# Kernel tuning notes

Hardware: AMD Instinct MI355X
Metric: run time of the kernel (lower is better)

## Reference

```python
import jax, jax.numpy as jnp
import numpy as np

B = 64; H = 56; W = 56; C = 128; NH = 4; WS = 7; SHIFT = 3; HID = 512
N = WS * WS            # tokens per window = 49
NW = (H // WS) * (W // WS)  # windows per image = 64
HD = C // NH           # head dim = 32


def _rel_index():
    # standard Swin relative-position index, [N, N] in [0, (2*WS-1)^2)
    coords = np.stack(np.meshgrid(np.arange(WS), np.arange(WS), indexing='ij'))  # [2,WS,WS]
    cf = coords.reshape(2, -1)
    rel = (cf[:, :, None] - cf[:, None, :]).transpose(1, 2, 0).astype(np.int64)  # [N,N,2]
    rel[:, :, 0] += WS - 1
    rel[:, :, 1] += WS - 1
    rel[:, :, 0] *= 2 * WS - 1
    return rel.sum(-1).astype(np.int32)


def _attn_mask():
    # standard Swin shifted-window mask, [NW, N, N] with 0 / -100
    img = np.zeros((H, W))
    cnt = 0
    sl = (slice(0, -WS), slice(-WS, -SHIFT), slice(-SHIFT, None))
    for hs in sl:
        for ws_ in sl:
            img[hs, ws_] = cnt
            cnt += 1
    mw = img.reshape(H // WS, WS, W // WS, WS).transpose(0, 2, 1, 3).reshape(-1, N)
    diff = mw[:, None, :] - mw[:, :, None]
    return np.where(diff != 0, -100.0, 0.0).astype(np.float32)


def setup_inputs() -> dict:
    key = jax.random.key(0)
    ks = jax.random.split(key, 12)
    s = 0.02
    return {
        'x': jax.random.normal(ks[0], (B, H * W, C), jnp.float32),
        'g1': jnp.ones((C,), jnp.float32),
        'b1': jnp.zeros((C,), jnp.float32),
        'w_qkv': jax.random.normal(ks[1], (C, 3 * C), jnp.float32) * s,
        'b_qkv': jnp.zeros((3 * C,), jnp.float32),
        'rel_bias': jax.random.normal(ks[2], ((2 * WS - 1) ** 2, NH), jnp.float32) * s,
        'w_proj': jax.random.normal(ks[3], (C, C), jnp.float32) * s,
        'b_proj': jnp.zeros((C,), jnp.float32),
        'g2': jnp.ones((C,), jnp.float32),
        'b2': jnp.zeros((C,), jnp.float32),
        'w_in': jax.random.normal(ks[4], (C, 2 * HID), jnp.float32) * s,
        'b_in': jnp.zeros((2 * HID,), jnp.float32),
        'w_core': jax.random.normal(ks[5], (HID, C), jnp.float32) * s,
        'b_core': jnp.zeros((C,), jnp.float32),
        'attn_mask': jnp.asarray(_attn_mask()),
        'rel_index': jnp.asarray(_rel_index()),
    }


def _ln(x, g, b, eps=1e-5):
    m = jnp.mean(x, axis=-1, keepdims=True)
    v = jnp.mean(jnp.square(x - m), axis=-1, keepdims=True)
    return (x - m) * jax.lax.rsqrt(v + eps) * g + b


def reference(x, g1, b1, w_qkv, b_qkv, rel_bias, w_proj, b_proj,
              g2, b2, w_in, b_in, w_core, b_core, attn_mask, rel_index):
    shortcut = x
    y = _ln(x, g1, b1).reshape(B, H, W, C)
    # cyclic shift
    y = jnp.roll(y, (-SHIFT, -SHIFT), axis=(1, 2))
    # window partition -> [B*NW, N, C]
    win = y.reshape(B, H // WS, WS, W // WS, WS, C).transpose(0, 1, 3, 2, 4, 5)
    win = win.reshape(B * NW, N, C)
    # qkv
    qkv = (win @ w_qkv + b_qkv).reshape(B * NW, N, 3, NH, HD).transpose(2, 0, 3, 1, 4)
    q, k, v = qkv[0], qkv[1], qkv[2]           # each [B*NW, NH, N, HD]
    scale = HD ** -0.5
    attn = jnp.einsum('bhqd,bhkd->bhqk', q * scale, k)   # [B*NW, NH, N, N]
    bias = rel_bias[rel_index]                  # [N, N, NH]
    attn = attn + bias.transpose(2, 0, 1)[None]
    # shifted-window mask
    attn = attn.reshape(B, NW, NH, N, N) + attn_mask[None, :, None]
    attn = jax.nn.softmax(attn.reshape(B * NW, NH, N, N), axis=-1)
    o = jnp.einsum('bhqk,bhkd->bhqd', attn, v).transpose(0, 2, 1, 3).reshape(B * NW, N, C)
    o = o @ w_proj + b_proj
    # window reverse + un-shift
    o = o.reshape(B, H // WS, W // WS, WS, WS, C).transpose(0, 1, 3, 2, 4, 5).reshape(B, H, W, C)
    o = jnp.roll(o, (SHIFT, SHIFT), axis=(1, 2)).reshape(B, H * W, C)
    x = shortcut + o
    # TM feed-forward (geglu gate path, continuous relaxation of the TM core)
    y = _ln(x, g2, b2)
    p = y @ w_in + b_in
    val, gate = jnp.split(p, 2, axis=-1)
    fused = jax.nn.gelu(val) * jax.nn.sigmoid(gate)
    out = fused @ w_core + b_core
    return x + out
```

## Files before the change

kernel.cpp:

```cpp
#include <hip/hip_runtime.h>
#include <hip/hip_bf16.h>


typedef unsigned short u16;
typedef __attribute__((ext_vector_type(8))) short short8;
typedef __attribute__((ext_vector_type(4))) float f32x4;

#define T_TOK 200704
#define CDIM  128
#define NTOK  49
#define WSZ   7
#define SHIFT 3
#define HID   512
#define PAD   136

__device__ __forceinline__ float bf2f(u16 v) {
    return __uint_as_float(((unsigned int)v) << 16);
}
__device__ __forceinline__ u16 f2bf(float f) {
    unsigned int u = __float_as_uint(f);
    unsigned int r = 0x7FFFu + ((u >> 16) & 1u);
    return (u16)((u + r) >> 16);
}

__global__ __launch_bounds__(256) void prep_weights(
    const float* __restrict__ w_qkv, const float* __restrict__ w_proj,
    const float* __restrict__ w_in,  const float* __restrict__ w_core,
    u16* __restrict__ qkvT, u16* __restrict__ projT,
    u16* __restrict__ inT,  u16* __restrict__ coreT)
{
    int g = blockIdx.x * 256 + threadIdx.x;
    if (g < 49152) {
        int k = g / 384, n = g % 384;
        qkvT[n * 128 + k] = f2bf(w_qkv[g]);
    } else if (g < 65536) {
        int h = g - 49152; int k = h / 128, n = h % 128;
        projT[n * 128 + k] = f2bf(w_proj[h]);
    } else if (g < 196608) {
        int h = g - 65536; int k = h / 1024, n = h % 1024;
        inT[n * 128 + k] = f2bf(w_in[h]);
    } else {
        int h = g - 196608; int k = h / 128, n = h % 128;
        coreT[n * 512 + k] = f2bf(w_core[h]);
    }
}

__global__ __launch_bounds__(256) void prep_combo(
    const float* __restrict__ mask, const float* __restrict__ rel_bias,
    const int* __restrict__ rel_index, u16* __restrict__ combo)
{
    int g = blockIdx.x * 256 + threadIdx.x;
    if (g >= 64 * 4 * 49 * 64) return;
    int kj = g & 63;
    int qi = (g >> 6) % 49;
    int head = (g / (64 * 49)) & 3;
    int w = g / (64 * 49 * 4);
    float v = 0.f;
    if (kj < 49) {
        int e = qi * 49 + kj;
        v = mask[w * 2401 + e] + rel_bias[rel_index[e] * 4 + head];
    }
    combo[g] = f2bf(v);
}

__global__ __launch_bounds__(256) void ln1_kernel(
    const float* __restrict__ xin, const float* __restrict__ gam,
    const float* __restrict__ bet, u16* __restrict__ outp)
{
    int wave = threadIdx.x >> 6, lane = threadIdx.x & 63;
    int t = blockIdx.x * 4 + wave;
    int win = t / NTOK, n = t - win * NTOK;
    int b = win >> 6, wi = win & 63;
    int hp = (wi >> 3) * WSZ + n / WSZ;
    int wp = (wi & 7) * WSZ + n % WSZ;
    int h = hp + SHIFT; if (h >= 56) h -= 56;
    int w = wp + SHIFT; if (w >= 56) w -= 56;
    int src = b * 3136 + h * 56 + w;
    const float* xr = xin + (size_t)src * CDIM;
    int c0 = lane * 2;
    float x0 = xr[c0], x1 = xr[c0 + 1];
    float s = x0 + x1;
    #pragma unroll
    for (int m = 1; m < 64; m <<= 1) s += __shfl_xor(s, m);
    float mean = s * (1.0f / 128.0f);
    float d0 = x0 - mean, d1 = x1 - mean;
    float v = d0 * d0 + d1 * d1;
    #pragma unroll
    for (int m = 1; m < 64; m <<= 1) v += __shfl_xor(v, m);
    float rstd = rsqrtf(v * (1.0f / 128.0f) + 1e-5f);
    float y0 = d0 * rstd * gam[c0]     + bet[c0];
    float y1 = d1 * rstd * gam[c0 + 1] + bet[c0 + 1];
    u16 pair[2] = { f2bf(y0), f2bf(y1) };
    *(unsigned int*)(outp + (size_t)t * CDIM + c0) = *(unsigned int*)pair;
}

__global__ __launch_bounds__(256) void ln2_kernel(
    const u16* __restrict__ xin, const float* __restrict__ gam,
    const float* __restrict__ bet, u16* __restrict__ outp)
{
    int wave = threadIdx.x >> 6, lane = threadIdx.x & 63;
    int t = blockIdx.x * 4 + wave;
    const u16* xr = xin + (size_t)t * CDIM;
    int c0 = lane * 2;
    float x0 = bf2f(xr[c0]), x1 = bf2f(xr[c0 + 1]);
    float s = x0 + x1;
    #pragma unroll
    for (int m = 1; m < 64; m <<= 1) s += __shfl_xor(s, m);
    float mean = s * (1.0f / 128.0f);
    float d0 = x0 - mean, d1 = x1 - mean;
    float v = d0 * d0 + d1 * d1;
    #pragma unroll
    for (int m = 1; m < 64; m <<= 1) v += __shfl_xor(v, m);
    float rstd = rsqrtf(v * (1.0f / 128.0f) + 1e-5f);
    float y0 = d0 * rstd * gam[c0]     + bet[c0];
    float y1 = d1 * rstd * gam[c0 + 1] + bet[c0 + 1];
    u16 pair[2] = { f2bf(y0), f2bf(y1) };
    *(unsigned int*)(outp + (size_t)t * CDIM + c0) = *(unsigned int*)pair;
}

__global__ __launch_bounds__(256) void qkv_gemm(
    const u16* __restrict__ A, const u16* __restrict__ WT,
    const float* __restrict__ bias,
    u16* __restrict__ qb, u16* __restrict__ kb, u16* __restrict__ vb)
{
    __shared__ __align__(16) short As[128 * PAD];
    __shared__ __align__(16) short Bs[64 * PAD];
    int tid = threadIdx.x;
    int m0 = blockIdx.x * 128;
    #pragma unroll
    for (int i = 0; i < 8; i++) {
        int e = i * 256 + tid; int row = e >> 4, c = e & 15;
        *(int4*)(As + row * PAD + c * 8) =
            *(const int4*)(A + (size_t)(m0 + row) * 128 + c * 8);
    }
    int w = tid >> 6, lane = tid & 63, lr = lane & 15, quad = lane >> 4;
    short8 af[2][4];
    const float scale = 0.17677669529663687f;
    for (int n0 = 0; n0 < 6; n0++) {
        #pragma unroll
        for (int i = 0; i < 4; i++) {
            int e = i * 256 + tid; int row = e >> 4, c = e & 15;
            *(int4*)(Bs + row * PAD + c * 8) =
                *(const int4*)(WT + (size_t)(n0 * 64 + row) * 128 + c * 8);
        }
        __syncthreads();
        if (n0 == 0) {
            #pragma unroll
            for (int mr = 0; mr < 2; mr++)
                #pragma unroll
                for (int ks = 0; ks < 4; ks++)
                    af[mr][ks] = *(const short8*)(As + (mr * 64 + w * 16 + lr) * PAD + ks * 32 + quad * 8);
        }
        f32x4 acc[8];
        #pragma unroll
        for (int i = 0; i < 8; i++) acc[i] = (f32x4){0.f, 0.f, 0.f, 0.f};
        #pragma unroll
        for (int ks = 0; ks < 4; ks++) {
            #pragma unroll
            for (int nt = 0; nt < 4; nt++) {
                short8 b = *(const short8*)(Bs + (nt * 16 + lr) * PAD + ks * 32 + quad * 8);
                acc[nt]     = __builtin_amdgcn_mfma_f32_16x16x32_bf16(af[0][ks], b, acc[nt], 0, 0, 0);
                acc[4 + nt] = __builtin_amdgcn_mfma_f32_16x16x32_bf16(af[1][ks], b, acc[4 + nt], 0, 0, 0);
            }
        }
        __syncthreads();
        #pragma unroll
        for (int nt = 0; nt < 4; nt++) {
            int col = n0 * 64 + nt * 16 + lr;
            int which = col >> 7, head = (col >> 5) & 3, hd = col & 31;
            u16* dst = (which == 0) ? qb : (which == 1 ? kb : vb);
            float bv = bias[col];
            #pragma unroll
            for (int mr = 0; mr < 2; mr++) {
                #pragma unroll
                for (int r = 0; r < 4; r++) {
                    int m = m0 + mr * 64 + w * 16 + quad * 4 + r;
                    int win = m / NTOK, n = m - win * NTOK;
                    float v = acc[mr * 4 + nt][r] + bv;
                    if (which == 0) v *= scale;
                    dst[(size_t)((win * 4 + head) * NTOK + n) * 32 + hd] = f2bf(v);
                }
            }
        }
    }
}

__global__ __launch_bounds__(256) void attn_kernel(
    const u16* __restrict__ qb, const u16* __restrict__ kb,
    const u16* __restrict__ vb, const u16* __restrict__ combo,
    u16* __restrict__ ob)
{
    __shared__ __align__(16) short Ps[4][64 * 72];
    __shared__ __align__(16) short Vt[4][32 * 72];
    int win = blockIdx.x;
    int w = threadIdx.x >> 6;
    int lane = threadIdx.x & 63;
    int lr = lane & 15, quad = lane >> 4;
    int wh = win * 4 + w;
    const u16* qp = qb + (size_t)wh * 1568;
    const u16* kp = kb + (size_t)wh * 1568;

    {
        const unsigned int* vp = (const unsigned int*)(vb + (size_t)wh * 1568);
        short* vt = Vt[w];
        for (int u = lane; u < 784; u += 64) {
            unsigned int v2 = vp[u];
            int kj = u >> 4, hd2 = (u & 15) * 2;
            vt[hd2 * 72 + kj]       = (short)(v2 & 0xffff);
            vt[(hd2 + 1) * 72 + kj] = (short)(v2 >> 16);
        }
    }

    short8 qa[4], kf[4];
    #pragma unroll
    for (int t = 0; t < 4; t++) {
        int row = t * 16 + lr;
        if (row < 49) {
            qa[t] = *(const short8*)(qp + row * 32 + quad * 8);
            kf[t] = *(const short8*)(kp + row * 32 + quad * 8);
        } else {
            qa[t] = (short8){0,0,0,0,0,0,0,0};
            kf[t] = (short8){0,0,0,0,0,0,0,0};
        }
    }

    f32x4 s[4][4];
    #pragma unroll
    for (int mt = 0; mt < 4; mt++)
        #pragma unroll
        for (int nt = 0; nt < 4; nt++)
            s[mt][nt] = (f32x4){0.f, 0.f, 0.f, 0.f};
    #pragma unroll
    for (int mt = 0; mt < 4; mt++)
        #pragma unroll
        for (int nt = 0; nt < 4; nt++)
            s[mt][nt] = __builtin_amdgcn_mfma_f32_16x16x32_bf16(qa[mt], kf[nt], s[mt][nt], 0, 0, 0);

    const u16* cb = combo + (size_t)(((win & 63) * 4 + w) * 49) * 64;
    short* ps = Ps[w];
    #pragma unroll
    for (int mt = 0; mt < 4; mt++) {
        #pragma unroll
        for (int r = 0; r < 4; r++) {
            int qi = mt * 16 + quad * 4 + r;
            float vv[4];
            #pragma unroll
            for (int nt = 0; nt < 4; nt++) {
                int kj = nt * 16 + lr;
                float val = s[mt][nt][r];
                if (kj < 49) {
                    if (qi < 49) val += bf2f(cb[qi * 64 + kj]);
                } else {
                    val = -1e30f;
                }
                vv[nt] = val;
            }
            float mx = fmaxf(fmaxf(vv[0], vv[1]), fmaxf(vv[2], vv[3]));
            #pragma unroll
            for (int msk = 1; msk < 16; msk <<= 1) mx = fmaxf(mx, __shfl_xor(mx, msk));
            float e[4], sum = 0.f;
            #pragma unroll
            for (int nt = 0; nt < 4; nt++) { e[nt] = __expf(vv[nt] - mx); sum += e[nt]; }
            #pragma unroll
            for (int msk = 1; msk < 16; msk <<= 1) sum += __shfl_xor(sum, msk);
            float inv = 1.f / sum;
            #pragma unroll
            for (int nt = 0; nt < 4; nt++)
                ps[qi * 72 + nt * 16 + lr] = (short)f2bf(e[nt] * inv);
        }
    }
    __syncthreads();

    short8 pa[4][2], vf[2][2];
    #pragma unroll
    for (int mt = 0; mt < 4; mt++)
        #pragma unroll
        for (int kc = 0; kc < 2; kc++)
            pa[mt][kc] = *(const short8*)(ps + (mt * 16 + lr) * 72 + kc * 32 + quad * 8);
    #pragma unroll
    for (int nt = 0; nt < 2; nt++)
        #pragma unroll
        for (int kc = 0; kc < 2; kc++)
            vf[nt][kc] = *(const short8*)(Vt[w] + (nt * 16 + lr) * 72 + kc * 32 + quad * 8);
    f32x4 o[4][2];
    #pragma unroll
    for (int mt = 0; mt < 4; mt++)
        #pragma unroll
        for (int nt = 0; nt < 2; nt++) {
            o[mt][nt] = (f32x4){0.f, 0.f, 0.f, 0.f};
            #pragma unroll
            for (int kc = 0; kc < 2; kc++)
                o[mt][nt] = __builtin_amdgcn_mfma_f32_16x16x32_bf16(pa[mt][kc], vf[nt][kc], o[mt][nt], 0, 0, 0);
        }

    #pragma unroll
    for (int mt = 0; mt < 4; mt++) {
        #pragma unroll
        for (int r = 0; r < 4; r++) {
            int qi = mt * 16 + quad * 4 + r;
            if (qi < 49) {
                u16* orow = ob + (size_t)(win * NTOK + qi) * CDIM + w * 32;
                #pragma unroll
                for (int nt = 0; nt < 2; nt++)
                    orow[nt * 16 + lr] = f2bf(o[mt][nt][r]);
            }
        }
    }
}

__global__ __launch_bounds__(256) void proj_gemm(
    const u16* __restrict__ A, const u16* __restrict__ WT,
    const float* __restrict__ bias, const float* __restrict__ xres,
    u16* __restrict__ x1)
{
    __shared__ __align__(16) short As[128 * PAD];
    __shared__ __align__(16) short Bs[64 * PAD];
    int tid = threadIdx.x;
    int m0 = blockIdx.x * 128;
    #pragma unroll
    for (int i = 0; i < 8; i++) {
        int e = i * 256 + tid; int row = e >> 4, c = e & 15;
        *(int4*)(As + row * PAD + c * 8) =
            *(const int4*)(A + (size_t)(m0 + row) * 128 + c * 8);
    }
    int w = tid >> 6, lane = tid & 63, lr = lane & 15, quad = lane >> 4;
    short8 af[2][4];
    for (int n0 = 0; n0 < 2; n0++) {
        #pragma unroll
        for (int i = 0; i < 4; i++) {
            int e = i * 256 + tid; int row = e >> 4, c = e & 15;
            *(int4*)(Bs + row * PAD + c * 8) =
                *(const int4*)(WT + (size_t)(n0 * 64 + row) * 128 + c * 8);
        }
        __syncthreads();
        if (n0 == 0) {
            #pragma unroll
            for (int mr = 0; mr < 2; mr++)
                #pragma unroll
                for (int ks = 0; ks < 4; ks++)
                    af[mr][ks] = *(const short8*)(As + (mr * 64 + w * 16 + lr) * PAD + ks * 32 + quad * 8);
        }
        f32x4 acc[8];
        #pragma unroll
        for (int i = 0; i < 8; i++) acc[i] = (f32x4){0.f, 0.f, 0.f, 0.f};
        #pragma unroll
        for (int ks = 0; ks < 4; ks++) {
            #pragma unroll
            for (int nt = 0; nt < 4; nt++) {
                short8 b = *(const short8*)(Bs + (nt * 16 + lr) * PAD + ks * 32 + quad * 8);
                acc[nt]     = __builtin_amdgcn_mfma_f32_16x16x32_bf16(af[0][ks], b, acc[nt], 0, 0, 0);
                acc[4 + nt] = __builtin_amdgcn_mfma_f32_16x16x32_bf16(af[1][ks], b, acc[4 + nt], 0, 0, 0);
            }
        }
        __syncthreads();
        #pragma unroll
        for (int nt = 0; nt < 4; nt++) {
            int col = n0 * 64 + nt * 16 + lr;
            float bv = bias[col];
            #pragma unroll
            for (int mr = 0; mr < 2; mr++) {
                #pragma unroll
                for (int r = 0; r < 4; r++) {
                    int m = m0 + mr * 64 + w * 16 + quad * 4 + r;
                    int win = m / NTOK, n = m - win * NTOK;
                    int b = win >> 6, wi = win & 63;
                    int hp = (wi >> 3) * WSZ + n / WSZ;
                    int wp = (wi & 7) * WSZ + n % WSZ;
                    int h = hp + SHIFT; if (h >= 56) h -= 56;
                    int ww = wp + SHIFT; if (ww >= 56) ww -= 56;
                    size_t tok = (size_t)b * 3136 + h * 56 + ww;
                    float v = acc[mr * 4 + nt][r] + bv + xres[tok * CDIM + col];
                    x1[tok * CDIM + col] = f2bf(v);
                }
            }
        }
    }
}

__global__ __launch_bounds__(256) void mlpin_gemm(
    const u16* __restrict__ A, const u16* __restrict__ WT,
    const float* __restrict__ bias, u16* __restrict__ fused)
{
    __shared__ __align__(16) short As[128 * PAD];
    __shared__ __align__(16) short Bs[64 * PAD];
    int tid = threadIdx.x;
    int m0 = blockIdx.x * 128;
    #pragma unroll
    for (int i = 0; i < 8; i++) {
        int e = i * 256 + tid; int row = e >> 4, c = e & 15;
        *(int4*)(As + row * PAD + c * 8) =
            *(const int4*)(A + (size_t)(m0 + row) * 128 + c * 8);
    }
    int w = tid >> 6, lane = tid & 63, lr = lane & 15, quad = lane >> 4;
    short8 af[2][4];
    for (int n0 = 0; n0 < 8; n0++) {
        #pragma unroll
        for (int i = 0; i < 4; i++) {
            int e = i * 256 + tid; int row = e >> 4, c = e & 15;
            *(int4*)(Bs + row * PAD + c * 8) =
                *(const int4*)(WT + (size_t)(n0 * 64 + row) * 128 + c * 8);
        }
        __syncthreads();
        if (n0 == 0) {
            #pragma unroll
            for (int mr = 0; mr < 2; mr++)
                #pragma unroll
                for (int ks = 0; ks < 4; ks++)
                    af[mr][ks] = *(const short8*)(As + (mr * 64 + w * 16 + lr) * PAD + ks * 32 + quad * 8);
        }
        f32x4 accv[8], accg[8];
        #pragma unroll
        for (int i = 0; i < 8; i++) accv[i] = (f32x4){0.f, 0.f, 0.f, 0.f};
        #pragma unroll
        for (int ks = 0; ks < 4; ks++) {
            #pragma unroll
            for (int nt = 0; nt < 4; nt++) {
                short8 b = *(const short8*)(Bs + (nt * 16 + lr) * PAD + ks * 32 + quad * 8);
                accv[nt]     = __builtin_amdgcn_mfma_f32_16x16x32_bf16(af[0][ks], b, accv[nt], 0, 0, 0);
                accv[4 + nt] = __builtin_amdgcn_mfma_f32_16x16x32_bf16(af[1][ks], b, accv[4 + nt], 0, 0, 0);
            }
        }
        __syncthreads();
        #pragma unroll
        for (int i = 0; i < 4; i++) {
            int e = i * 256 + tid; int row = e >> 4, c = e & 15;
            *(int4*)(Bs + row * PAD + c * 8) =
                *(const int4*)(WT + (size_t)(512 + n0 * 64 + row) * 128 + c * 8);
        }
        __syncthreads();
        #pragma unroll
        for (int i = 0; i < 8; i++) accg[i] = (f32x4){0.f, 0.f, 0.f, 0.f};
        #pragma unroll
        for (int ks = 0; ks < 4; ks++) {
            #pragma unroll
            for (int nt = 0; nt < 4; nt++) {
                short8 b = *(const short8*)(Bs + (nt * 16 + lr) * PAD + ks * 32 + quad * 8);
                accg[nt]     = __builtin_amdgcn_mfma_f32_16x16x32_bf16(af[0][ks], b, accg[nt], 0, 0, 0);
                accg[4 + nt] = __builtin_amdgcn_mfma_f32_16x16x32_bf16(af[1][ks], b, accg[4 + nt], 0, 0, 0);
            }
        }
        __syncthreads();
        #pragma unroll
        for (int nt = 0; nt < 4; nt++) {
            int col = n0 * 64 + nt * 16 + lr;
            float bv = bias[col];
            float bg = bias[512 + col];
            #pragma unroll
            for (int mr = 0; mr < 2; mr++) {
                #pragma unroll
                for (int r = 0; r < 4; r++) {
                    int m = m0 + mr * 64 + w * 16 + quad * 4 + r;
                    float x = accv[mr * 4 + nt][r] + bv;
                    float g = accg[mr * 4 + nt][r] + bg;
                    float t = tanhf(0.7978845608028654f * (x + 0.044715f * x * x * x));
                    float gel = 0.5f * x * (1.f + t);
                    float sig = 1.f / (1.f + __expf(-g));
                    fused[(size_t)m * HID + col] = f2bf(gel * sig);
                }
            }
        }
    }
}

__global__ __launch_bounds__(256) void mlpcore_gemm(
    const u16* __restrict__ A, const u16* __restrict__ WT,
    const float* __restrict__ bias, const u16* __restrict__ x1,
    float* __restrict__ outp)
{
    __shared__ __align__(16) short As[128 * PAD];
    __shared__ __align__(16) short Bs[64 * PAD];
    int tid = threadIdx.x;
    int m0 = blockIdx.x * 128;
    int w = tid >> 6, lane = tid & 63, lr = lane & 15, quad = lane >> 4;
    f32x4 acc[16];
    #pragma unroll
    for (int i = 0; i < 16; i++) acc[i] = (f32x4){0.f, 0.f, 0.f, 0.f};
    for (int kc = 0; kc < 4; kc++) {
        #pragma unroll
        for (int i = 0; i < 8; i++) {
            int e = i * 256 + tid; int row = e >> 4, c = e & 15;
            *(int4*)(As + row * PAD + c * 8) =
                *(const int4*)(A + (size_t)(m0 + row) * HID + kc * 128 + c * 8);
        }
        #pragma unroll
        for (int i = 0; i < 4; i++) {
            int e = i * 256 + tid; int row = e >> 4, c = e & 15;
            *(int4*)(Bs + row * PAD + c * 8) =
                *(const int4*)(WT + (size_t)row * 512 + kc * 128 + c * 8);
        }
        __syncthreads();
        short8 af[2][4];
        #pragma unroll
        for (int mr = 0; mr < 2; mr++)
            #pragma unroll
            for (int ks = 0; ks < 4; ks++)
                af[mr][ks] = *(const short8*)(As + (mr * 64 + w * 16 + lr) * PAD + ks * 32 + quad * 8);
        #pragma unroll
        for (int ks = 0; ks < 4; ks++) {
            #pragma unroll
            for (int nt = 0; nt < 4; nt++) {
                short8 b = *(const short8*)(Bs + (nt * 16 + lr) * PAD + ks * 32 + quad * 8);
                acc[nt]     = __builtin_amdgcn_mfma_f32_16x16x32_bf16(af[0][ks], b, acc[nt], 0, 0, 0);
                acc[4 + nt] = __builtin_amdgcn_mfma_f32_16x16x32_bf16(af[1][ks], b, acc[4 + nt], 0, 0, 0);
            }
        }
        __syncthreads();
        #pragma unroll
        for (int i = 0; i < 4; i++) {
            int e = i * 256 + tid; int row = e >> 4, c = e & 15;
            *(int4*)(Bs + row * PAD + c * 8) =
                *(const int4*)(WT + (size_t)(64 + row) * 512 + kc * 128 + c * 8);
        }
        __syncthreads();
        #pragma unroll
        for (int ks = 0; ks < 4; ks++) {
            #pragma unroll
            for (int nt = 0; nt < 4; nt++) {
                short8 b = *(const short8*)(Bs + (nt * 16 + lr) * PAD + ks * 32 + quad * 8);
                acc[8 + nt]  = __builtin_amdgcn_mfma_f32_16x16x32_bf16(af[0][ks], b, acc[8 + nt], 0, 0, 0);
                acc[12 + nt] = __builtin_amdgcn_mfma_f32_16x16x32_bf16(af[1][ks], b, acc[12 + nt], 0, 0, 0);
            }
        }
        __syncthreads();
    }
    #pragma unroll
    for (int n0 = 0; n0 < 2; n0++) {
        #pragma unroll
        for (int nt = 0; nt < 4; nt++) {
            int col = n0 * 64 + nt * 16 + lr;
            float bv = bias[col];
            #pragma unroll
            for (int mr = 0; mr < 2; mr++) {
                #pragma unroll
                for (int r = 0; r < 4; r++) {
                    int m = m0 + mr * 64 + w * 16 + quad * 4 + r;
                    float v = acc[n0 * 8 + mr * 4 + nt][r] + bv + bf2f(x1[(size_t)m * CDIM + col]);
                    outp[(size_t)m * CDIM + col] = v;
                }
            }
        }
    }
}

extern "C" void kernel_launch(void* const* d_in, const int* in_sizes, int n_in,
                              void* d_out, int out_size, void* d_ws, size_t ws_size,
                              hipStream_t stream)
{
    const float* x        = (const float*)d_in[0];
    const float* g1       = (const float*)d_in[1];
    const float* b1       = (const float*)d_in[2];
    const float* w_qkv    = (const float*)d_in[3];
    const float* b_qkv    = (const float*)d_in[4];
    const float* rel_bias = (const float*)d_in[5];
    const float* w_proj   = (const float*)d_in[6];
    const float* b_proj   = (const float*)d_in[7];
    const float* g2       = (const float*)d_in[8];
    const float* b2       = (const float*)d_in[9];
    const float* w_in     = (const float*)d_in[10];
    const float* b_in     = (const float*)d_in[11];
    const float* w_core   = (const float*)d_in[12];
    const float* b_core   = (const float*)d_in[13];
    const float* attn_mask = (const float*)d_in[14];
    const int*   rel_index = (const int*)d_in[15];
    float* outp = (float*)d_out;

    char* ws = (char*)d_ws;
    const size_t sz128 = (size_t)T_TOK * CDIM * sizeof(u16);
    u16* qb    = (u16*)(ws);
    u16* kb    = (u16*)(ws + sz128);
    u16* vb    = (u16*)(ws + 2 * sz128);
    u16* ob    = (u16*)(ws + 3 * sz128);
    u16* fused = (u16*)(ws);
    u16* ybuf  = (u16*)(ws + 4 * sz128);
    u16* x1    = (u16*)(ws + 5 * sz128);
    u16* combo = x1;
    u16* qkvT  = (u16*)(ws + 6 * sz128);
    u16* projT = (u16*)(ws + 6 * sz128 + 98304);
    u16* inT   = (u16*)(ws + 6 * sz128 + 131072);
    u16* coreT = (u16*)(ws + 6 * sz128 + 393216);

    prep_weights<<<1024, 256, 0, stream>>>(w_qkv, w_proj, w_in, w_core,
                                           qkvT, projT, inT, coreT);
    prep_combo<<<3136, 256, 0, stream>>>(attn_mask, rel_bias, rel_index, combo);
    ln1_kernel<<<T_TOK / 4, 256, 0, stream>>>(x, g1, b1, ybuf);
    qkv_gemm<<<T_TOK / 128, 256, 0, stream>>>(ybuf, qkvT, b_qkv, qb, kb, vb);
    attn_kernel<<<4096, 256, 0, stream>>>(qb, kb, vb, combo, ob);
    proj_gemm<<<T_TOK / 128, 256, 0, stream>>>(ob, projT, b_proj, x, x1);
    ln2_kernel<<<T_TOK / 4, 256, 0, stream>>>(x1, g2, b2, ybuf);
    mlpin_gemm<<<T_TOK / 128, 256, 0, stream>>>(ybuf, inT, b_in, fused);
    mlpcore_gemm<<<T_TOK / 128, 256, 0, stream>>>(fused, coreT, b_core, x1, outp);
}
```

Before: 850.6 us.

## Fuse MLP input GEMM, GEGLU gate and core GEMM into one kernel

```diff
diff --git a/kernel.cpp b/kernel.cpp
--- a/kernel.cpp
+++ b/kernel.cpp
@@ -13,6 +13,7 @@
 #define SHIFT 3
 #define HID   512
 #define PAD   136
+#define FPAD  516
 
 __device__ __forceinline__ float bf2f(u16 v) {
     return __uint_as_float(((unsigned int)v) << 16);
@@ -377,166 +378,93 @@
     }
 }
 
-__global__ __launch_bounds__(256) void mlpin_gemm(
-    const u16* __restrict__ A, const u16* __restrict__ WT,
-    const float* __restrict__ bias, u16* __restrict__ fused)
-{
-    __shared__ __align__(16) short As[128 * PAD];
-    __shared__ __align__(16) short Bs[64 * PAD];
+__global__ __launch_bounds__(256) void mlp_fused(
+    const u16* __restrict__ A, const u16* __restrict__ inT,
+    const u16* __restrict__ coreT, const float* __restrict__ b_in,
+    const float* __restrict__ b_core, const u16* __restrict__ x1,
+    float* __restrict__ outp)
+{
+    __shared__ __align__(16) short Fs[64 * FPAD];
     int tid = threadIdx.x;
-    int m0 = blockIdx.x * 128;
-    #pragma unroll
-    for (int i = 0; i < 8; i++) {
-        int e = i * 256 + tid; int row = e >> 4, c = e & 15;
-        *(int4*)(As + row * PAD + c * 8) =
-            *(const int4*)(A + (size_t)(m0 + row) * 128 + c * 8);
-    }
+    int m0 = blockIdx.x * 64;
     int w = tid >> 6, lane = tid & 63, lr = lane & 15, quad = lane >> 4;
-    short8 af[2][4];
-    for (int n0 = 0; n0 < 8; n0++) {
-        #pragma unroll
-        for (int i = 0; i < 4; i++) {
-            int e = i * 256 + tid; int row = e >> 4, c = e & 15;
-            *(int4*)(Bs + row * PAD + c * 8) =
-                *(const int4*)(WT + (size_t)(n0 * 64 + row) * 128 + c * 8);
-        }
-        __syncthreads();
-        if (n0 == 0) {
-            #pragma unroll
-            for (int mr = 0; mr < 2; mr++)
-                #pragma unroll
-                for (int ks = 0; ks < 4; ks++)
-                    af[mr][ks] = *(const short8*)(As + (mr * 64 + w * 16 + lr) * PAD + ks * 32 + quad * 8);
-        }
-        f32x4 accv[8], accg[8];
-        #pragma unroll
-        for (int i = 0; i < 8; i++) accv[i] = (f32x4){0.f, 0.f, 0.f, 0.f};
+
+    short8 af[4][4];
+    #pragma unroll
+    for (int mt = 0; mt < 4; mt++)
+        #pragma unroll
+        for (int ks = 0; ks < 4; ks++)
+            af[mt][ks] = *(const short8*)(A + (size_t)(m0 + mt * 16 + lr) * 128 + ks * 32 + quad * 8);
+
+    #pragma unroll 2
+    for (int j = 0; j < 8; j++) {
+        int colv = w * 128 + j * 16 + lr;
+        short8 bv[4], bg[4];
         #pragma unroll
         for (int ks = 0; ks < 4; ks++) {
-            #pragma unroll
-            for (int nt = 0; nt < 4; nt++) {
-                short8 b = *(const short8*)(Bs + (nt * 16 + lr) * PAD + ks * 32 + quad * 8);
-                accv[nt]     = __builtin_amdgcn_mfma_f32_16x16x32_bf16(af[0][ks], b, accv[nt], 0, 0, 0);
-                accv[4 + nt] = __builtin_amdgcn_mfma_f32_16x16x32_bf16(af[1][ks], b, accv[4 + nt], 0, 0, 0);
-            }
-        }
-        __syncthreads();
-        #pragma unroll
-        for (int i = 0; i < 4; i++) {
-            int e = i * 256 + tid; int row = e >> 4, c = e & 15;
-            *(int4*)(Bs + row * PAD + c * 8) =
-                *(const int4*)(WT + (size_t)(512 + n0 * 64 + row) * 128 + c * 8);
-        }
-        __syncthreads();
-        #pragma unroll
-        for (int i = 0; i < 8; i++) accg[i] = (f32x4){0.f, 0.f, 0.f, 0.f};
-        #pragma unroll
-        for (int ks = 0; ks < 4; ks++) {
-            #pragma unroll
-            for (int nt = 0; nt < 4; nt++) {
-                short8 b = *(const short8*)(Bs + (nt * 16 + lr) * PAD + ks * 32 + quad * 8);
-                accg[nt]     = __builtin_amdgcn_mfma_f32_16x16x32_bf16(af[0][ks], b, accg[nt], 0, 0, 0);
-                accg[4 + nt] = __builtin_amdgcn_mfma_f32_16x16x32_bf16(af[1][ks], b, accg[4 + nt], 0, 0, 0);
-            }
-        }
-        __syncthreads();
-        #pragma unroll
-        for (int nt = 0; nt < 4; nt++) {
-            int col = n0 * 64 + nt * 16 + lr;
-            float bv = bias[col];
-            float bg = bias[512 + col];
-            #pragma unroll
-            for (int mr = 0; mr < 2; mr++) {
-                #pragma unroll
-                for (int r = 0; r < 4; r++) {
-                    int m = m0 + mr * 64 + w * 16 + quad * 4 + r;
-                    float x = accv[mr * 4 + nt][r] + bv;
-                    float g = accg[mr * 4 + nt][r] + bg;
-                    float t = tanhf(0.7978845608028654f * (x + 0.044715f * x * x * x));
-                    float gel = 0.5f * x * (1.f + t);
-                    float sig = 1.f / (1.f + __expf(-g));
-                    fused[(size_t)m * HID + col] = f2bf(gel * sig);
-                }
-            }
-        }
-    }
-}
-
-__global__ __launch_bounds__(256) void mlpcore_gemm(
-    const u16* __restrict__ A, const u16* __restrict__ WT,
-    const float* __restrict__ bias, const u16* __restrict__ x1,
-    float* __restrict__ outp)
-{
-    __shared__ __align__(16) short As[128 * PAD];
-    __shared__ __align__(16) short Bs[64 * PAD];
-    int tid = threadIdx.x;
-    int m0 = blockIdx.x * 128;
-    int w = tid >> 6, lane = tid & 63, lr = lane & 15, quad = lane >> 4;
-    f32x4 acc[16];
-    #pragma unroll
-    for (int i = 0; i < 16; i++) acc[i] = (f32x4){0.f, 0.f, 0.f, 0.f};
-    for (int kc = 0; kc < 4; kc++) {
-        #pragma unroll
-        for (int i = 0; i < 8; i++) {
-            int e = i * 256 + tid; int row = e >> 4, c = e & 15;
-            *(int4*)(As + row * PAD + c * 8) =
-                *(const int4*)(A + (size_t)(m0 + row) * HID + kc * 128 + c * 8);
-        }
-        #pragma unroll
-        for (int i = 0; i < 4; i++) {
-            int e = i * 256 + tid; int row = e >> 4, c = e & 15;
-            *(int4*)(Bs + row * PAD + c * 8) =
-                *(const int4*)(WT + (size_t)row * 512 + kc * 128 + c * 8);
-        }
-        __syncthreads();
-        short8 af[2][4];
-        #pragma unroll
-        for (int mr = 0; mr < 2; mr++)
-            #pragma unroll
-            for (int ks = 0; ks < 4; ks++)
-                af[mr][ks] = *(const short8*)(As + (mr * 64 + w * 16 + lr) * PAD + ks * 32 + quad * 8);
-        #pragma unroll
-        for (int ks = 0; ks < 4; ks++) {
-            #pragma unroll
-            for (int nt = 0; nt < 4; nt++) {
-                short8 b = *(const short8*)(Bs + (nt * 16 + lr) * PAD + ks * 32 + quad * 8);
-                acc[nt]     = __builtin_amdgcn_mfma_f32_16x16x32_bf16(af[0][ks], b, acc[nt], 0, 0, 0);
-                acc[4 + nt] = __builtin_amdgcn_mfma_f32_16x16x32_bf16(af[1][ks], b, acc[4 + nt], 0, 0, 0);
-            }
-        }
-        __syncthreads();
-        #pragma unroll
-        for (int i = 0; i < 4; i++) {
-            int e = i * 256 + tid; int row = e >> 4, c = e & 15;
-            *(int4*)(Bs + row * PAD + c * 8) =
-                *(const int4*)(WT + (size_t)(64 + row) * 512 + kc * 128 + c * 8);
-        }
-        __syncthreads();
-        #pragma unroll
-        for (int ks = 0; ks < 4; ks++) {
-            #pragma unroll
-            for (int nt = 0; nt < 4; nt++) {
-                short8 b = *(const short8*)(Bs + (nt * 16 + lr) * PAD + ks * 32 + quad * 8);
-                acc[8 + nt]  = __builtin_amdgcn_mfma_f32_16x16x32_bf16(af[0][ks], b, acc[8 + nt], 0, 0, 0);
-                acc[12 + nt] = __builtin_amdgcn_mfma_f32_16x16x32_bf16(af[1][ks], b, acc[12 + nt], 0, 0, 0);
-            }
-        }
-        __syncthreads();
-    }
-    #pragma unroll
-    for (int n0 = 0; n0 < 2; n0++) {
-        #pragma unroll
-        for (int nt = 0; nt < 4; nt++) {
-            int col = n0 * 64 + nt * 16 + lr;
-            float bv = bias[col];
-            #pragma unroll
-            for (int mr = 0; mr < 2; mr++) {
-                #pragma unroll
-                for (int r = 0; r < 4; r++) {
-                    int m = m0 + mr * 64 + w * 16 + quad * 4 + r;
-                    float v = acc[n0 * 8 + mr * 4 + nt][r] + bv + bf2f(x1[(size_t)m * CDIM + col]);
-                    outp[(size_t)m * CDIM + col] = v;
-                }
+            bv[ks] = *(const short8*)(inT + (size_t)colv * 128 + ks * 32 + quad * 8);
+            bg[ks] = *(const short8*)(inT + (size_t)(512 + colv) * 128 + ks * 32 + quad * 8);
+        }
+        float bvb = b_in[colv], bgb = b_in[512 + colv];
+        f32x4 accv[4], accg[4];
+        #pragma unroll
+        for (int mt = 0; mt < 4; mt++) {
+            accv[mt] = (f32x4){0.f, 0.f, 0.f, 0.f};
+            accg[mt] = (f32x4){0.f, 0.f, 0.f, 0.f};
+        }
+        #pragma unroll
+        for (int ks = 0; ks < 4; ks++)
+            #pragma unroll
+            for (int mt = 0; mt < 4; mt++) {
+                accv[mt] = __builtin_amdgcn_mfma_f32_16x16x32_bf16(af[mt][ks], bv[ks], accv[mt], 0, 0, 0);
+                accg[mt] = __builtin_amdgcn_mfma_f32_16x16x32_bf16(af[mt][ks], bg[ks], accg[mt], 0, 0, 0);
+            }
+        #pragma unroll
+        for (int mt = 0; mt < 4; mt++) {
+            #pragma unroll
+            for (int r = 0; r < 4; r++) {
+                float xv = accv[mt][r] + bvb;
+                float g  = accg[mt][r] + bgb;
+                float z2 = 1.5957691216057308f * (xv + 0.044715f * xv * xv * xv);
+                float gel = xv / (1.f + __expf(-z2));
+                float sig = 1.f / (1.f + __expf(-g));
+                Fs[(mt * 16 + quad * 4 + r) * FPAD + colv] = (short)f2bf(gel * sig);
+            }
+        }
+    }
+    __syncthreads();
+
+    f32x4 o[4][2];
+    #pragma unroll
+    for (int mt = 0; mt < 4; mt++)
+        #pragma unroll
+        for (int nt = 0; nt < 2; nt++)
+            o[mt][nt] = (f32x4){0.f, 0.f, 0.f, 0.f};
+    #pragma unroll 4
+    for (int ks = 0; ks < 16; ks++) {
+        short8 bf[2];
+        #pragma unroll
+        for (int nt = 0; nt < 2; nt++)
+            bf[nt] = *(const short8*)(coreT + (size_t)(w * 32 + nt * 16 + lr) * 512 + ks * 32 + quad * 8);
+        #pragma unroll
+        for (int mt = 0; mt < 4; mt++) {
+            short8 a2 = *(const short8*)(Fs + (mt * 16 + lr) * FPAD + ks * 32 + quad * 8);
+            o[mt][0] = __builtin_amdgcn_mfma_f32_16x16x32_bf16(a2, bf[0], o[mt][0], 0, 0, 0);
+            o[mt][1] = __builtin_amdgcn_mfma_f32_16x16x32_bf16(a2, bf[1], o[mt][1], 0, 0, 0);
+        }
+    }
+
+    #pragma unroll
+    for (int nt = 0; nt < 2; nt++) {
+        int col = w * 32 + nt * 16 + lr;
+        float bv = b_core[col];
+        #pragma unroll
+        for (int mt = 0; mt < 4; mt++) {
+            #pragma unroll
+            for (int r = 0; r < 4; r++) {
+                int m = m0 + mt * 16 + quad * 4 + r;
+                float v = o[mt][nt][r] + bv + bf2f(x1[(size_t)m * CDIM + col]);
+                outp[(size_t)m * CDIM + col] = v;
             }
         }
     }
@@ -570,7 +498,6 @@
     u16* kb    = (u16*)(ws + sz128);
     u16* vb    = (u16*)(ws + 2 * sz128);
     u16* ob    = (u16*)(ws + 3 * sz128);
-    u16* fused = (u16*)(ws);
     u16* ybuf  = (u16*)(ws + 4 * sz128);
     u16* x1    = (u16*)(ws + 5 * sz128);
     u16* combo = x1;
@@ -587,6 +514,5 @@
     attn_kernel<<<4096, 256, 0, stream>>>(qb, kb, vb, combo, ob);
     proj_gemm<<<T_TOK / 128, 256, 0, stream>>>(ob, projT, b_proj, x, x1);
     ln2_kernel<<<T_TOK / 4, 256, 0, stream>>>(x1, g2, b2, ybuf);
-    mlpin_gemm<<<T_TOK / 128, 256, 0, stream>>>(ybuf, inT, b_in, fused);
-    mlpcore_gemm<<<T_TOK / 128, 256, 0, stream>>>(fused, coreT, b_core, x1, outp);
-}
+    mlp_fused<<<T_TOK / 64, 256, 0, stream>>>(ybuf, inT, coreT, b_in, b_core, x1, outp);
+}
```

After: 698.9 us (median of 2 runs). 17.8% less time.
